# Kernel optimization log

Measured on AMD Instinct MI355X. Metric: run time of the kernel, lower is better.

## Reference

```python
import jax, jax.numpy as jnp
import numpy as np

N = 50000       # num_nodes
E = 800000      # num_edges (avg degree 16)
DIN = 128       # input_dim
DOUT = 128      # output_dim
H = 4           # num_heads
HD = DOUT // H  # head_dim = 32


def setup_inputs() -> dict:
    key = jax.random.key(0)
    ks = jax.random.split(key, 9)
    x = jax.random.normal(ks[0], (N, DIN), dtype=jnp.float32)
    edge_index = jax.random.randint(ks[1], (2, E), 0, N, dtype=jnp.int64)
    s = 1.0 / np.sqrt(DIN)
    Wq = jax.random.uniform(ks[2], (DOUT, DIN), jnp.float32, -s, s)
    bq = jax.random.uniform(ks[3], (DOUT,), jnp.float32, -s, s)
    Wk = jax.random.uniform(ks[4], (DOUT, DIN), jnp.float32, -s, s)
    bk = jax.random.uniform(ks[5], (DOUT,), jnp.float32, -s, s)
    Wv = jax.random.uniform(ks[6], (DOUT, DIN), jnp.float32, -s, s)
    bv = jax.random.uniform(ks[7], (DOUT,), jnp.float32, -s, s)
    att = jax.random.normal(ks[8], (H, 2 * HD), dtype=jnp.float32)  # nn.Parameter(randn)
    return {"x": x, "edge_index": edge_index, "Wq": Wq, "bq": bq,
            "Wk": Wk, "bk": bk, "Wv": Wv, "bv": bv, "att": att}


def reference(x, edge_index, Wq, bq, Wk, bk, Wv, bv, att):
    n = x.shape[0]
    q = (x @ Wq.T + bq).reshape(n, H, HD)
    k = (x @ Wk.T + bk).reshape(n, H, HD)
    v = (x @ Wv.T + bv).reshape(n, H, HD)
    row, col = edge_index[0], edge_index[1]

    # scores = leaky_relu(sum(cat([q[row],k[col]]) * att)) computed without concat
    a_q, a_k = att[:, :HD], att[:, HD:]                       # [H,HD] each
    scores = jnp.einsum('ehd,hd->eh', q[row], a_q) \
           + jnp.einsum('ehd,hd->eh', k[col], a_k)            # [E,H]
    scores = jax.nn.leaky_relu(scores, 0.2)

    # segment-softmax over edges grouped by destination node (col), per head
    m = jax.ops.segment_max(scores, col, num_segments=n)      # [N,H]
    m = jnp.where(jnp.isfinite(m), m, 0.0)                    # empty segments -> -inf guard
    e = jnp.exp(scores - m[col])                              # [E,H]
    denom = jax.ops.segment_sum(e, col, num_segments=n)       # [N,H]
    w_edge = e / denom[col]                                   # softmax per dst segment

    # attention_weights[i] = mean over incoming edges of softmax weights; 0 if deg==0
    deg = jax.ops.segment_sum(jnp.ones((col.shape[0],), jnp.float32), col,
                              num_segments=n)                 # [N]
    w_sum = jax.ops.segment_sum(w_edge, col, num_segments=n)  # [N,H]
    attn_w = jnp.where(deg[:, None] > 0, w_sum / jnp.maximum(deg, 1.0)[:, None], 0.0)

    # output[dst] += attn_w[dst] * v[src], summed over edges
    msgs = attn_w[col][:, :, None] * v[row]                   # [E,H,HD]
    out = jax.ops.segment_sum(msgs, col, num_segments=n)      # [N,H,HD]
    return out.reshape(n, DOUT)                               # dropout: eval mode (identity)
```

## Files before the change

kernel.cpp:

```cpp
#include <hip/hip_runtime.h>


#define N_NODES 50000
#define N_EDGES 800000
#define SPAN    48
#define NBUCK   1042
#define CAP     1152
#define EPB     2048
#define NCHUNK  391

#define OFF_SORTED 12800000
#define OFF_CURSOR 17601536

typedef __attribute__((ext_vector_type(8))) short short8;
typedef __attribute__((ext_vector_type(4))) float f32x4;

__device__ __forceinline__ unsigned int pack_bf16_rne(float a, float b) {
    unsigned int ua = __float_as_uint(a), ub = __float_as_uint(b);
    unsigned int ha = (ua + 0x7FFFu + ((ua >> 16) & 1u)) >> 16;
    unsigned int hb = (ub + 0x7FFFu + ((ub >> 16) & 1u)) >> 16;
    return ha | (hb << 16);
}
__device__ __forceinline__ unsigned short bf16_rne(float a) {
    unsigned int ua = __float_as_uint(a);
    return (unsigned short)((ua + 0x7FFFu + ((ua >> 16) & 1u)) >> 16);
}
__device__ __forceinline__ float bflo(unsigned int u) { return __uint_as_float(u << 16); }
__device__ __forceinline__ float bfhi(unsigned int u) { return __uint_as_float(u & 0xFFFF0000u); }

__global__ __launch_bounds__(512) void gemm_v(const float* __restrict__ x,
                                              const float* __restrict__ Wv,
                                              const float* __restrict__ bv,
                                              unsigned int* __restrict__ vh) {
    __shared__ __align__(16) unsigned int wB[128 * 68];
    int t = threadIdx.x;

    for (int q = t; q < 8192; q += 512) {
        int o = q >> 6, k2 = q & 63;
        float2 wp = ((const float2*)Wv)[q];
        wB[o * 68 + k2] = pack_bf16_rne(wp.x, wp.y);
    }
    __syncthreads();

    int lane = t & 63, w = t >> 6;
    int quad = lane >> 4, lc = lane & 15;
    int n0 = blockIdx.x * 128 + w * 16;

    int arow = n0 + lc;
    int arowc = min(arow, N_NODES - 1);
    const float4* xrow = (const float4*)(x + (size_t)arowc * 128);

    f32x4 acc[8];
    #pragma unroll
    for (int ot = 0; ot < 8; ++ot) acc[ot] = (f32x4){0.f, 0.f, 0.f, 0.f};

    #pragma unroll
    for (int ks = 0; ks < 4; ++ks) {
        float4 f0 = xrow[ks * 8 + quad * 2];
        float4 f1 = xrow[ks * 8 + quad * 2 + 1];
        uint4 a4;
        a4.x = pack_bf16_rne(f0.x, f0.y);
        a4.y = pack_bf16_rne(f0.z, f0.w);
        a4.z = pack_bf16_rne(f1.x, f1.y);
        a4.w = pack_bf16_rne(f1.z, f1.w);
        short8 af = *(const short8*)&a4;
        #pragma unroll
        for (int ot = 0; ot < 8; ++ot) {
            uint4 b4 = *(const uint4*)&wB[(ot * 16 + lc) * 68 + ks * 16 + quad * 4];
            short8 bf = *(const short8*)&b4;
            acc[ot] = __builtin_amdgcn_mfma_f32_16x16x32_bf16(af, bf, acc[ot], 0, 0, 0);
        }
    }

    #pragma unroll
    for (int ot = 0; ot < 8; ++ot) {
        int o = ot * 16 + lc;
        float bb = bv[o];
        #pragma unroll
        for (int r = 0; r < 4; ++r) {
            int node = n0 + quad * 4 + r;
            unsigned short u = bf16_rne(acc[ot][r] + bb);
            unsigned int partner = (unsigned int)__shfl_xor((int)u, 1, 64);
            if ((lane & 1) == 0 && node < N_NODES) {
                unsigned int pair = (unsigned int)u | (partner << 16);
                vh[(size_t)node * 64 + (o >> 1)] = pair;
            }
        }
    }
}

__global__ __launch_bounds__(512) void scatter_kernel(const int* __restrict__ ei,
                                                      int* __restrict__ Cursor,
                                                      unsigned int* __restrict__ sorted) {
    __shared__ unsigned int w[EPB];
    __shared__ int h[NBUCK];
    __shared__ int base[NBUCK];
    __shared__ int s_wide;
    int t = threadIdx.x;
    for (int j = t; j < NBUCK; j += 512) h[j] = 0;
    if (t < 64) {
        int nz = (ei[2 * t + 1] != 0) ? 1 : 0;
        unsigned long long b = __ballot(nz);
        if (t == 0) s_wide = (b == 0ULL) ? 1 : 0;
    }
    __syncthreads();
    int wide = s_wide;
    int e0 = blockIdx.x * EPB;

    #pragma unroll
    for (int k = 0; k < EPB / 512; ++k) {
        int e = e0 + k * 512 + t;
        if (e < N_EDGES) {
            int r = wide ? ei[2 * e] : ei[e];
            int c = wide ? ei[2 * (N_EDGES + e)] : ei[N_EDGES + e];
            w[k * 512 + t] = ((unsigned int)c << 16) | (unsigned int)r;
            atomicAdd(&h[c / SPAN], 1);
        } else {
            w[k * 512 + t] = 0xFFFFFFFFu;
        }
    }
    __syncthreads();
    for (int j = t; j < NBUCK; j += 512) {
        int cnt = h[j];
        base[j] = cnt ? atomicAdd(&Cursor[j], cnt) : 0;
        h[j] = 0;
    }
    __syncthreads();
    #pragma unroll
    for (int k = 0; k < EPB / 512; ++k) {
        unsigned int ww = w[k * 512 + t];
        if (ww != 0xFFFFFFFFu) {
            int bin = (int)(ww >> 16) / SPAN;
            int p = base[bin] + atomicAdd(&h[bin], 1);
            if (p < CAP)
                sorted[(size_t)bin * CAP + p] = ww;
        }
    }
}

__global__ __launch_bounds__(256) void gather_kernel(const unsigned int* __restrict__ vh,
                                                     const unsigned int* __restrict__ sorted,
                                                     const int* __restrict__ Cursor,
                                                     float* __restrict__ out) {
    __shared__ unsigned int ww[CAP];
    __shared__ unsigned short rl[CAP];
    __shared__ int deg[SPAN];
    __shared__ int startc[SPAN];
    __shared__ int curp[SPAN];
    __shared__ int sc_s[64];
    int t = threadIdx.x;
    int b = blockIdx.x;
    int nb0 = b * SPAN;
    int span = min(SPAN, N_NODES - nb0);
    int cnt = min(Cursor[b], CAP);
    if (t < SPAN) deg[t] = 0;
    __syncthreads();

    const unsigned int* run = sorted + (size_t)b * CAP;
    for (int i = t; i < cnt; i += 256) {
        unsigned int v = run[i];
        ww[i] = v;
        atomicAdd(&deg[(int)(v >> 16) - nb0], 1);
    }
    __syncthreads();

    if (t < 64) sc_s[t] = (t < SPAN) ? deg[t] : 0;
    __syncthreads();
    for (int off = 1; off < 64; off <<= 1) {
        int y = (t < 64 && t >= off) ? sc_s[t - off] : 0;
        __syncthreads();
        if (t < 64) sc_s[t] += y;
        __syncthreads();
    }
    if (t < SPAN) { startc[t] = sc_s[t] - deg[t]; curp[t] = 0; }
    __syncthreads();

    for (int i = t; i < cnt; i += 256) {
        unsigned int v = ww[i];
        int ln = (int)(v >> 16) - nb0;
        int p = startc[ln] + atomicAdd(&curp[ln], 1);
        rl[p] = (unsigned short)(v & 0xFFFFu);
    }
    __syncthreads();

    int lane = t & 63, wid = t >> 6;
    int half = lane >> 5;
    int li = lane & 31;
    const uint2* v2 = (const uint2*)vh;

    for (int ln = wid; ln < span; ln += 4) {
        int s0 = startc[ln], d = deg[ln];
        double c0a = 0., c1a = 0., c2a = 0., c3a = 0.;
        double c0b = 0., c1b = 0., c2b = 0., c3b = 0.;
        int j = 0;
        for (; j + 8 <= d; j += 8) {
            int rA0 = rl[s0 + j + 0], rB0 = rl[s0 + j + 1];
            int rA1 = rl[s0 + j + 2], rB1 = rl[s0 + j + 3];
            int rA2 = rl[s0 + j + 4], rB2 = rl[s0 + j + 5];
            int rA3 = rl[s0 + j + 6], rB3 = rl[s0 + j + 7];
            uint2 p0 = v2[(size_t)(half ? rB0 : rA0) * 32 + li];
            uint2 p1 = v2[(size_t)(half ? rB1 : rA1) * 32 + li];
            uint2 p2 = v2[(size_t)(half ? rB2 : rA2) * 32 + li];
            uint2 p3 = v2[(size_t)(half ? rB3 : rA3) * 32 + li];
            c0a += (double)bflo(p0.x); c1a += (double)bfhi(p0.x);
            c2a += (double)bflo(p0.y); c3a += (double)bfhi(p0.y);
            c0b += (double)bflo(p1.x); c1b += (double)bfhi(p1.x);
            c2b += (double)bflo(p1.y); c3b += (double)bfhi(p1.y);
            c0a += (double)bflo(p2.x); c1a += (double)bfhi(p2.x);
            c2a += (double)bflo(p2.y); c3a += (double)bfhi(p2.y);
            c0b += (double)bflo(p3.x); c1b += (double)bfhi(p3.x);
            c2b += (double)bflo(p3.y); c3b += (double)bfhi(p3.y);
        }
        for (; j + 2 <= d; j += 2) {
            int rA = rl[s0 + j], rB = rl[s0 + j + 1];
            uint2 p0 = v2[(size_t)(half ? rB : rA) * 32 + li];
            c0a += (double)bflo(p0.x); c1a += (double)bfhi(p0.x);
            c2a += (double)bflo(p0.y); c3a += (double)bfhi(p0.y);
        }
        if (j < d) {
            int rA = rl[s0 + j];
            uint2 p0 = v2[(size_t)rA * 32 + li];
            if (!half) {
                c0a += (double)bflo(p0.x); c1a += (double)bfhi(p0.x);
                c2a += (double)bflo(p0.y); c3a += (double)bfhi(p0.y);
            }
        }
        double c0 = c0a + c0b, c1 = c1a + c1b, c2 = c2a + c2b, c3 = c3a + c3b;
        c0 += __shfl_xor(c0, 32, 64);
        c1 += __shfl_xor(c1, 32, 64);
        c2 += __shfl_xor(c2, 32, 64);
        c3 += __shfl_xor(c3, 32, 64);
        if (half == 0) {
            double sc = (d > 0) ? 1.0 / (double)d : 0.0;
            float4 res = {(float)(c0 * sc), (float)(c1 * sc),
                          (float)(c2 * sc), (float)(c3 * sc)};
            ((float4*)out)[(size_t)(nb0 + ln) * 32 + li] = res;
        }
    }
}

extern "C" void kernel_launch(void* const* d_in, const int* in_sizes, int n_in,
                              void* d_out, int out_size, void* d_ws, size_t ws_size,
                              hipStream_t stream) {
    const float* x  = (const float*)d_in[0];
    const int*   ei = (const int*)d_in[1];
    const float* Wv = (const float*)d_in[6];
    const float* bv = (const float*)d_in[7];
    float* out = (float*)d_out;

    char* ws = (char*)d_ws;
    unsigned int* vh     = (unsigned int*)(ws);
    unsigned int* sorted = (unsigned int*)(ws + OFF_SORTED);
    int*          Cursor = (int*)(ws + OFF_CURSOR);

    hipMemsetAsync(Cursor, 0, NBUCK * sizeof(int), stream);
    gemm_v<<<(N_NODES + 127) / 128, 512, 0, stream>>>(x, Wv, bv, vh);
    scatter_kernel<<<NCHUNK, 512, 0, stream>>>(ei, Cursor, sorted);
    gather_kernel<<<NBUCK, 256, 0, stream>>>(vh, sorted, Cursor, out);
}
```

Before: 154.9 us.

## Fuse GEMM and edge scatter into one launch, widen gather buckets to 96 nodes

Merges the V-projection GEMM and the edge bucketing scatter into a single kernel whose blocks pick a role by block index, so both phases run concurrently in one launch. The bucket span doubles to 96 nodes (521 buckets, capacity 2304), and the gather kernel moves to 512 threads to match. The 64-bit edge index read becomes a uint2 load. This removes one launch and lets the memory-bound scatter overlap the GEMM. In exchange, the gather runs fewer, larger blocks, which may lower occupancy. The larger bucket capacity also has to fit within the workspace offsets.

```diff
diff --git a/kernel.cpp b/kernel.cpp
--- a/kernel.cpp
+++ b/kernel.cpp
@@ -3,11 +3,12 @@
 
 #define N_NODES 50000
 #define N_EDGES 800000
-#define SPAN    48
-#define NBUCK   1042
-#define CAP     1152
+#define SPAN    96
+#define NBUCK   521
+#define CAP     2304
 #define EPB     2048
 #define NCHUNK  391
+#define GEMMB   391
 
 #define OFF_SORTED 12800000
 #define OFF_CURSOR 17601536
@@ -28,117 +29,122 @@
 __device__ __forceinline__ float bflo(unsigned int u) { return __uint_as_float(u << 16); }
 __device__ __forceinline__ float bfhi(unsigned int u) { return __uint_as_float(u & 0xFFFF0000u); }
 
-__global__ __launch_bounds__(512) void gemm_v(const float* __restrict__ x,
-                                              const float* __restrict__ Wv,
-                                              const float* __restrict__ bv,
-                                              unsigned int* __restrict__ vh) {
-    __shared__ __align__(16) unsigned int wB[128 * 68];
-    int t = threadIdx.x;
-
-    for (int q = t; q < 8192; q += 512) {
-        int o = q >> 6, k2 = q & 63;
-        float2 wp = ((const float2*)Wv)[q];
-        wB[o * 68 + k2] = pack_bf16_rne(wp.x, wp.y);
-    }
-    __syncthreads();
-
-    int lane = t & 63, w = t >> 6;
-    int quad = lane >> 4, lc = lane & 15;
-    int n0 = blockIdx.x * 128 + w * 16;
-
-    int arow = n0 + lc;
-    int arowc = min(arow, N_NODES - 1);
-    const float4* xrow = (const float4*)(x + (size_t)arowc * 128);
-
-    f32x4 acc[8];
-    #pragma unroll
-    for (int ot = 0; ot < 8; ++ot) acc[ot] = (f32x4){0.f, 0.f, 0.f, 0.f};
-
-    #pragma unroll
-    for (int ks = 0; ks < 4; ++ks) {
-        float4 f0 = xrow[ks * 8 + quad * 2];
-        float4 f1 = xrow[ks * 8 + quad * 2 + 1];
-        uint4 a4;
-        a4.x = pack_bf16_rne(f0.x, f0.y);
-        a4.y = pack_bf16_rne(f0.z, f0.w);
-        a4.z = pack_bf16_rne(f1.x, f1.y);
-        a4.w = pack_bf16_rne(f1.z, f1.w);
-        short8 af = *(const short8*)&a4;
-        #pragma unroll
-        for (int ot = 0; ot < 8; ++ot) {
-            uint4 b4 = *(const uint4*)&wB[(ot * 16 + lc) * 68 + ks * 16 + quad * 4];
-            short8 bf = *(const short8*)&b4;
-            acc[ot] = __builtin_amdgcn_mfma_f32_16x16x32_bf16(af, bf, acc[ot], 0, 0, 0);
-        }
-    }
-
-    #pragma unroll
-    for (int ot = 0; ot < 8; ++ot) {
-        int o = ot * 16 + lc;
-        float bb = bv[o];
-        #pragma unroll
-        for (int r = 0; r < 4; ++r) {
-            int node = n0 + quad * 4 + r;
-            unsigned short u = bf16_rne(acc[ot][r] + bb);
-            unsigned int partner = (unsigned int)__shfl_xor((int)u, 1, 64);
-            if ((lane & 1) == 0 && node < N_NODES) {
-                unsigned int pair = (unsigned int)u | (partner << 16);
-                vh[(size_t)node * 64 + (o >> 1)] = pair;
-            }
-        }
-    }
-}
-
-__global__ __launch_bounds__(512) void scatter_kernel(const int* __restrict__ ei,
-                                                      int* __restrict__ Cursor,
-                                                      unsigned int* __restrict__ sorted) {
-    __shared__ unsigned int w[EPB];
-    __shared__ int h[NBUCK];
-    __shared__ int base[NBUCK];
+__global__ __launch_bounds__(512) void fused_gemm_scatter(
+        const float* __restrict__ x, const float* __restrict__ Wv,
+        const float* __restrict__ bv, unsigned int* __restrict__ vh,
+        const int* __restrict__ ei, int* __restrict__ Cursor,
+        unsigned int* __restrict__ sorted) {
+    __shared__ __align__(16) unsigned char smem[128 * 68 * 4];
     __shared__ int s_wide;
     int t = threadIdx.x;
-    for (int j = t; j < NBUCK; j += 512) h[j] = 0;
-    if (t < 64) {
-        int nz = (ei[2 * t + 1] != 0) ? 1 : 0;
-        unsigned long long b = __ballot(nz);
-        if (t == 0) s_wide = (b == 0ULL) ? 1 : 0;
-    }
-    __syncthreads();
-    int wide = s_wide;
-    int e0 = blockIdx.x * EPB;
-
-    #pragma unroll
-    for (int k = 0; k < EPB / 512; ++k) {
-        int e = e0 + k * 512 + t;
-        if (e < N_EDGES) {
-            int r = wide ? ei[2 * e] : ei[e];
-            int c = wide ? ei[2 * (N_EDGES + e)] : ei[N_EDGES + e];
-            w[k * 512 + t] = ((unsigned int)c << 16) | (unsigned int)r;
-            atomicAdd(&h[c / SPAN], 1);
-        } else {
-            w[k * 512 + t] = 0xFFFFFFFFu;
-        }
-    }
-    __syncthreads();
-    for (int j = t; j < NBUCK; j += 512) {
-        int cnt = h[j];
-        base[j] = cnt ? atomicAdd(&Cursor[j], cnt) : 0;
-        h[j] = 0;
-    }
-    __syncthreads();
-    #pragma unroll
-    for (int k = 0; k < EPB / 512; ++k) {
-        unsigned int ww = w[k * 512 + t];
-        if (ww != 0xFFFFFFFFu) {
-            int bin = (int)(ww >> 16) / SPAN;
-            int p = base[bin] + atomicAdd(&h[bin], 1);
-            if (p < CAP)
-                sorted[(size_t)bin * CAP + p] = ww;
-        }
-    }
-}
-
-__global__ __launch_bounds__(256) void gather_kernel(const unsigned int* __restrict__ vh,
+
+    if (blockIdx.x < GEMMB) {
+        unsigned int* wB = (unsigned int*)smem;
+        for (int q = t; q < 8192; q += 512) {
+            int o = q >> 6, k2 = q & 63;
+            float2 wp = ((const float2*)Wv)[q];
+            wB[o * 68 + k2] = pack_bf16_rne(wp.x, wp.y);
+        }
+        __syncthreads();
+
+        int lane = t & 63, w = t >> 6;
+        int quad = lane >> 4, lc = lane & 15;
+        int n0 = blockIdx.x * 128 + w * 16;
+
+        int arow = n0 + lc;
+        int arowc = min(arow, N_NODES - 1);
+        const float4* xrow = (const float4*)(x + (size_t)arowc * 128);
+
+        f32x4 acc[8];
+        #pragma unroll
+        for (int ot = 0; ot < 8; ++ot) acc[ot] = (f32x4){0.f, 0.f, 0.f, 0.f};
+
+        #pragma unroll
+        for (int ks = 0; ks < 4; ++ks) {
+            float4 f0 = xrow[ks * 8 + quad * 2];
+            float4 f1 = xrow[ks * 8 + quad * 2 + 1];
+            uint4 a4;
+            a4.x = pack_bf16_rne(f0.x, f0.y);
+            a4.y = pack_bf16_rne(f0.z, f0.w);
+            a4.z = pack_bf16_rne(f1.x, f1.y);
+            a4.w = pack_bf16_rne(f1.z, f1.w);
+            short8 af = *(const short8*)&a4;
+            #pragma unroll
+            for (int ot = 0; ot < 8; ++ot) {
+                uint4 b4 = *(const uint4*)&wB[(ot * 16 + lc) * 68 + ks * 16 + quad * 4];
+                short8 bf = *(const short8*)&b4;
+                acc[ot] = __builtin_amdgcn_mfma_f32_16x16x32_bf16(af, bf, acc[ot], 0, 0, 0);
+            }
+        }
+
+        #pragma unroll
+        for (int ot = 0; ot < 8; ++ot) {
+            int o = ot * 16 + lc;
+            float bb = bv[o];
+            #pragma unroll
+            for (int r = 0; r < 4; ++r) {
+                int node = n0 + quad * 4 + r;
+                unsigned short u = bf16_rne(acc[ot][r] + bb);
+                unsigned int partner = (unsigned int)__shfl_xor((int)u, 1, 64);
+                if ((lane & 1) == 0 && node < N_NODES) {
+                    unsigned int pair = (unsigned int)u | (partner << 16);
+                    vh[(size_t)node * 64 + (o >> 1)] = pair;
+                }
+            }
+        }
+    } else {
+        unsigned int* w = (unsigned int*)smem;
+        int* h    = (int*)(smem + EPB * 4);
+        int* base = (int*)(smem + EPB * 4 + NBUCK * 4);
+        for (int j = t; j < NBUCK; j += 512) h[j] = 0;
+        if (t < 64) {
+            int nz = (ei[2 * t + 1] != 0) ? 1 : 0;
+            unsigned long long b = __ballot(nz);
+            if (t == 0) s_wide = (b == 0ULL) ? 1 : 0;
+        }
+        __syncthreads();
+        int wide = s_wide;
+        int e0 = (blockIdx.x - GEMMB) * EPB;
+
+        #pragma unroll
+        for (int k = 0; k < EPB / 512; ++k) {
+            int e = e0 + k * 512 + t;
+            if (e < N_EDGES) {
+                int r, c;
+                if (wide) {
+                    r = (int)((const uint2*)ei)[e].x;
+                    c = (int)((const uint2*)ei)[N_EDGES + e].x;
+                } else {
+                    r = ei[e];
+                    c = ei[N_EDGES + e];
+                }
+                w[k * 512 + t] = ((unsigned int)c << 16) | (unsigned int)r;
+                atomicAdd(&h[c / SPAN], 1);
+            } else {
+                w[k * 512 + t] = 0xFFFFFFFFu;
+            }
+        }
+        __syncthreads();
+        for (int j = t; j < NBUCK; j += 512) {
+            int cnt = h[j];
+            base[j] = cnt ? atomicAdd(&Cursor[j], cnt) : 0;
+            h[j] = 0;
+        }
+        __syncthreads();
+        #pragma unroll
+        for (int k = 0; k < EPB / 512; ++k) {
+            unsigned int ww = w[k * 512 + t];
+            if (ww != 0xFFFFFFFFu) {
+                int bin = (int)(ww >> 16) / SPAN;
+                int p = base[bin] + atomicAdd(&h[bin], 1);
+                if (p < CAP)
+                    sorted[(size_t)bin * CAP + p] = ww;
+            }
+        }
+    }
+}
+
+__global__ __launch_bounds__(512) void gather_kernel(const unsigned int* __restrict__ vh,
                                                      const unsigned int* __restrict__ sorted,
                                                      const int* __restrict__ Cursor,
                                                      float* __restrict__ out) {
@@ -147,7 +153,7 @@
     __shared__ int deg[SPAN];
     __shared__ int startc[SPAN];
     __shared__ int curp[SPAN];
-    __shared__ int sc_s[64];
+    __shared__ int sc_s[128];
     int t = threadIdx.x;
     int b = blockIdx.x;
     int nb0 = b * SPAN;
@@ -157,25 +163,25 @@
     __syncthreads();
 
     const unsigned int* run = sorted + (size_t)b * CAP;
-    for (int i = t; i < cnt; i += 256) {
+    for (int i = t; i < cnt; i += 512) {
         unsigned int v = run[i];
         ww[i] = v;
         atomicAdd(&deg[(int)(v >> 16) - nb0], 1);
     }
     __syncthreads();
 
-    if (t < 64) sc_s[t] = (t < SPAN) ? deg[t] : 0;
-    __syncthreads();
-    for (int off = 1; off < 64; off <<= 1) {
-        int y = (t < 64 && t >= off) ? sc_s[t - off] : 0;
-        __syncthreads();
-        if (t < 64) sc_s[t] += y;
+    if (t < 128) sc_s[t] = (t < SPAN) ? deg[t] : 0;
+    __syncthreads();
+    for (int off = 1; off < 128; off <<= 1) {
+        int y = (t < 128 && t >= off) ? sc_s[t - off] : 0;
+        __syncthreads();
+        if (t < 128) sc_s[t] += y;
         __syncthreads();
     }
     if (t < SPAN) { startc[t] = sc_s[t] - deg[t]; curp[t] = 0; }
     __syncthreads();
 
-    for (int i = t; i < cnt; i += 256) {
+    for (int i = t; i < cnt; i += 512) {
         unsigned int v = ww[i];
         int ln = (int)(v >> 16) - nb0;
         int p = startc[ln] + atomicAdd(&curp[ln], 1);
@@ -188,7 +194,7 @@
     int li = lane & 31;
     const uint2* v2 = (const uint2*)vh;
 
-    for (int ln = wid; ln < span; ln += 4) {
+    for (int ln = wid; ln < span; ln += 8) {
         int s0 = startc[ln], d = deg[ln];
         double c0a = 0., c1a = 0., c2a = 0., c3a = 0.;
         double c0b = 0., c1b = 0., c2b = 0., c3b = 0.;
@@ -254,7 +260,7 @@
     int*          Cursor = (int*)(ws + OFF_CURSOR);
 
     hipMemsetAsync(Cursor, 0, NBUCK * sizeof(int), stream);
-    gemm_v<<<(N_NODES + 127) / 128, 512, 0, stream>>>(x, Wv, bv, vh);
-    scatter_kernel<<<NCHUNK, 512, 0, stream>>>(ei, Cursor, sorted);
-    gather_kernel<<<NBUCK, 256, 0, stream>>>(vh, sorted, Cursor, out);
-}
+    fused_gemm_scatter<<<GEMMB + NCHUNK, 512, 0, stream>>>(x, Wv, bv, vh,
+                                                           ei, Cursor, sorted);
+    gather_kernel<<<NBUCK, 512, 0, stream>>>(vh, sorted, Cursor, out);
+}
```

Measured after the change: 146.5 us. 5.4% less time.
